# Optimization experiments

Hardware: AMD Instinct MI355X
Metric: run time of the kernel (lower is better)

The kernel has to match this reference:

```python
import jax, jax.numpy as jnp
import numpy as np

N_IN = 1024
N_OUT = 1024
BATCH = 8192
N_GRID = 10  # grid_points = linspace(-1, 1, 10); 9 segments
LN_EPS = 1e-5


def setup_inputs() -> dict:
    key = jax.random.key(0)
    k = jax.random.split(key, 6)
    return {
        "x": jax.random.normal(k[0], (BATCH, N_IN), dtype=jnp.float32),
        "weights": jax.random.normal(k[1], (N_OUT, N_IN), dtype=jnp.float32) * (1.0 / np.sqrt(N_IN)),
        "biases": jax.random.normal(k[2], (N_OUT,), dtype=jnp.float32),
        "slopes": jax.random.normal(k[3], (N_OUT, N_IN, N_GRID - 1), dtype=jnp.float32) * 0.05,
        "intercepts": jax.random.normal(k[4], (N_OUT, N_IN, N_GRID - 1), dtype=jnp.float32) * 0.05,
        "prelu_weight": jnp.full((1,), 0.25, dtype=jnp.float32),
    }


def reference(x, weights, biases, slopes, intercepts, prelu_weight):
    grid = jnp.linspace(-1.0, 1.0, N_GRID, dtype=x.dtype)
    n_seg = N_GRID - 1

    # base branch: GELU (exact, matching torch nn.GELU default) then linear
    b_out = jax.nn.gelu(x, approximate=False) @ weights.T + biases  # [B, n_out]

    # segment index per (sample, input feature)
    pos = (x[..., None] - grid) >= 0  # [B, n_in, N_GRID]
    seg = jnp.clip(jnp.sum(pos.astype(jnp.int32), axis=-1) - 1, 0, n_seg - 1)  # [B, n_in]

    # Faithful to torch.gather semantics: only slopes[:, 0, :] / intercepts[:, 0, :]
    # are read (index dim-2 has size 1 -> j==0). The piecewise sum over n_in then
    # reduces to segment-sums of x and segment counts contracted with those slices.
    onehot = jax.nn.one_hot(seg, n_seg, dtype=x.dtype)  # [B, n_in, n_seg]
    seg_x = jnp.einsum('bis,bi->bs', onehot, x)          # sum of x per segment
    seg_cnt = jnp.sum(onehot, axis=1)                    # count per segment
    slopes0 = slopes[:, 0, :]        # [n_out, n_seg]
    icpt0 = intercepts[:, 0, :]      # [n_out, n_seg]
    lin = seg_x @ slopes0.T + seg_cnt @ icpt0.T          # [B, n_out]

    y = b_out + lin
    # LayerNorm over n_out, no affine
    mu = jnp.mean(y, axis=-1, keepdims=True)
    var = jnp.mean(jnp.square(y - mu), axis=-1, keepdims=True)
    yn = (y - mu) * jax.lax.rsqrt(var + LN_EPS)
    # PReLU with single shared weight
    return jnp.where(yn >= 0, yn, prelu_weight * yn)
```

## Files before the change

### kernel.cpp

```cpp
#include <hip/hip_runtime.h>
#include <hip/hip_fp8.h>

#define N_IN 1024
#define N_OUT 1024
#define BATCHN 8192

typedef __attribute__((ext_vector_type(4))) int intx4;
typedef __attribute__((ext_vector_type(8))) int intx8;
typedef __attribute__((ext_vector_type(16))) float floatx16;

__device__ __forceinline__ unsigned int pk4_e4m3(float a, float b, float c,
                                                 float d) {
  int w = __builtin_amdgcn_cvt_pk_fp8_f32(a, b, 0, false);
  w = __builtin_amdgcn_cvt_pk_fp8_f32(c, d, w, true);
  return (unsigned int)w;
}
__device__ __forceinline__ float gelu_fast(float v) {
  float e = __builtin_amdgcn_exp2f(-2.4554443f * v);
  return v * __builtin_amdgcn_rcpf(1.0f + e);
}

__global__ __launch_bounds__(256) void prep_w(const float* __restrict__ W,
                                              unsigned char* __restrict__ Wb8,
                                              const float* __restrict__ slopes,
                                              const float* __restrict__ icpts,
                                              float* __restrict__ slt,
                                              float* __restrict__ ict) {
  const int b = blockIdx.x, t = threadIdx.x;
  if (b < N_OUT) {
    const int o = b;
    float4 v = ((const float4*)(W + o * N_IN))[t];
    unsigned int pk =
        pk4_e4m3(v.x * 16.0f, v.y * 16.0f, v.z * 16.0f, v.w * 16.0f);
    const int kc = t >> 4;
    const int lh = (t >> 3) & 1;
    const int sec = (t >> 2) & 1;
    const int off = (t & 3) * 4;
    const int lane = lh * 32 + (o & 31);
    *(unsigned int*)(Wb8 + kc * 65536 + (o >> 5) * 2048 + sec * 1024 +
                     lane * 16 + off) = pk;
  } else {
    const int gb = b - N_OUT;
    const int o = gb * 16 + (t >> 4);
    const int s = t & 15;
    if (s < 9) {
      slt[s * N_OUT + o] = slopes[(long)o * 9216 + s];
      ict[s * N_OUT + o] = icpts[(long)o * 9216 + s];
    }
  }
}

__global__ __launch_bounds__(1024) void fused(const float* __restrict__ x,
                                              const unsigned char* __restrict__ Wb8,
                                              const float* __restrict__ biases,
                                              const float* __restrict__ slt,
                                              const float* __restrict__ ict,
                                              const float* __restrict__ prelu_w,
                                              float* __restrict__ out) {
  __shared__ unsigned char lA[32 * 1024];
  __shared__ float2 seg2[32][12];
  __shared__ float2 red[16][32];
  __shared__ float2 rowstat[32];

  const int t = threadIdx.x;
  const int lane = t & 63, w = t >> 6;
  const int l31 = lane & 31, lh = lane >> 5;
  const int r0 = blockIdx.x * 32;

  for (int jr = 0; jr < 2; ++jr) {
    const int rl = 2 * w + jr;
    const float* xr = x + (r0 + rl) * N_IN;
    unsigned int* lrow = (unsigned int*)(lA + rl * 1024);
    const int sw = rl & 7;
    float cum[8], cumx[8], totx = 0.f;
#pragma unroll
    for (int s = 0; s < 8; ++s) { cum[s] = 0.f; cumx[s] = 0.f; }
#pragma unroll
    for (int jc = 0; jc < 4; ++jc) {
      float4 v4 = ((const float4*)xr)[lane + 64 * jc];
      float vs[4] = {v4.x, v4.y, v4.z, v4.w};
      float gs[4];
#pragma unroll
      for (int e = 0; e < 4; ++e) {
        float v = vs[e];
        gs[e] = gelu_fast(v) * 4.0f;
        totx += v;
#pragma unroll
        for (int k = 0; k < 8; ++k) {
          bool m = v >= (-1.0f + (float)(k + 1) * (2.0f / 9.0f));
          cum[k] += m ? 1.0f : 0.0f;
          cumx[k] += m ? v : 0.0f;
        }
      }
      const unsigned int pk = pk4_e4m3(gs[0], gs[1], gs[2], gs[3]);
      const int d = lane + 64 * jc;
      lrow[(((d >> 2) ^ sw) << 2) | (d & 3)] = pk;
    }
#pragma unroll
    for (int off = 32; off > 0; off >>= 1) {
      totx += __shfl_xor(totx, off);
#pragma unroll
      for (int s = 0; s < 8; ++s) {
        cum[s] += __shfl_xor(cum[s], off);
        cumx[s] += __shfl_xor(cumx[s], off);
      }
    }
    if (lane == 0) {
      seg2[rl][0] = make_float2(totx - cumx[0], 1024.f - cum[0]);
#pragma unroll
      for (int s = 1; s < 8; ++s)
        seg2[rl][s] = make_float2(cumx[s - 1] - cumx[s], cum[s - 1] - cum[s]);
      seg2[rl][8] = make_float2(cumx[7], cum[7]);
    }
  }
  __syncthreads();

  const int nb = w * 64;
  floatx16 acc[2] = {};
  const unsigned char* aRow = lA + l31 * 1024;
  const int asw = l31 & 7;
  const unsigned char* bBase = Wb8 + (w * 2) * 2048 + lane * 16;

#define LOAD_A(ko, AF)                                                         \
  {                                                                            \
    const int c0 = ((ko) >> 4) + lh * 2;                                       \
    intx4 lo = *(const intx4*)(aRow + ((c0 ^ asw) << 4));                      \
    intx4 hi = *(const intx4*)(aRow + (((c0 + 1) ^ asw) << 4));                \
    AF[0] = lo[0]; AF[1] = lo[1]; AF[2] = lo[2]; AF[3] = lo[3];                \
    AF[4] = hi[0]; AF[5] = hi[1]; AF[6] = hi[2]; AF[7] = hi[3];                \
  }
#define LOAD_B(kc, ni, BF)                                                     \
  {                                                                            \
    const unsigned char* bp = bBase + (kc) * 65536 + (ni) * 2048;              \
    intx4 lo = *(const intx4*)bp;                                              \
    intx4 hi = *(const intx4*)(bp + 1024);                                     \
    BF[0] = lo[0]; BF[1] = lo[1]; BF[2] = lo[2]; BF[3] = lo[3];                \
    BF[4] = hi[0]; BF[5] = hi[1]; BF[6] = hi[2]; BF[7] = hi[3];                \
  }

  const int rot = ((blockIdx.x >> 3) & 7) * 2;
  for (int kt0 = 0; kt0 < 16; kt0 += 2) {
    const int kt = (kt0 + rot) & 15;
    intx8 a0, a1, b0[2], b1[2];
    LOAD_A(kt * 64, a0);
    LOAD_A(kt * 64 + 64, a1);
#pragma unroll
    for (int ni = 0; ni < 2; ++ni) LOAD_B(kt, ni, b0[ni]);
#pragma unroll
    for (int ni = 0; ni < 2; ++ni) LOAD_B(kt + 1, ni, b1[ni]);
    __builtin_amdgcn_s_setprio(1);
#pragma unroll
    for (int ni = 0; ni < 2; ++ni)
      acc[ni] = __builtin_amdgcn_mfma_scale_f32_32x32x64_f8f6f4(
          a0, b0[ni], acc[ni], 0, 0, 0, 0x7D7D7D7Du , 0,
          0x7B7B7B7Bu );
#pragma unroll
    for (int ni = 0; ni < 2; ++ni)
      acc[ni] = __builtin_amdgcn_mfma_scale_f32_32x32x64_f8f6f4(
          a1, b1[ni], acc[ni], 0, 0, 0, 0x7D7D7D7Du, 0, 0x7B7B7B7Bu);
    __builtin_amdgcn_s_setprio(0);
  }

  float bb[2], cs[2][9], ci[2][9];
#pragma unroll
  for (int ni = 0; ni < 2; ++ni) {
    const int c = nb + ni * 32 + l31;
    bb[ni] = biases[c];
#pragma unroll
    for (int s = 0; s < 9; ++s) {
      cs[ni][s] = slt[s * N_OUT + c];
      ci[ni][s] = ict[s * N_OUT + c];
    }
  }

#pragma unroll
  for (int rg = 0; rg < 16; ++rg) {
    const int rl = (rg & 3) + 8 * (rg >> 2) + 4 * lh;
    float2 sp[9];
#pragma unroll
    for (int s = 0; s < 9; ++s) sp[s] = seg2[rl][s];
    float ssum = 0.f, qsum = 0.f;
#pragma unroll
    for (int ni = 0; ni < 2; ++ni) {
      float y = acc[ni][rg] + bb[ni];
#pragma unroll
      for (int s = 0; s < 9; ++s) y += sp[s].x * cs[ni][s] + sp[s].y * ci[ni][s];
      acc[ni][rg] = y;
      ssum += y;
      qsum += y * y;
    }
#pragma unroll
    for (int off = 16; off > 0; off >>= 1) {
      ssum += __shfl_xor(ssum, off);
      qsum += __shfl_xor(qsum, off);
    }
    if (l31 == 0) red[w][rl] = make_float2(ssum, qsum);
  }
  __syncthreads();
  if (t < 32) {
    float s = 0.f, q = 0.f;
#pragma unroll
    for (int wv = 0; wv < 16; ++wv) {
      float2 p = red[wv][t];
      s += p.x;
      q += p.y;
    }
    const float mu = s * (1.0f / 1024.0f);
    const float rstd = rsqrtf(q * (1.0f / 1024.0f) - mu * mu + 1e-5f);
    rowstat[t] = make_float2(mu, rstd);
  }
  const float pw = prelu_w[0];
  __syncthreads();
#pragma unroll
  for (int rg = 0; rg < 16; ++rg) {
    const int rl = (rg & 3) + 8 * (rg >> 2) + 4 * lh;
    const float2 ms = rowstat[rl];
    float* orow = out + (r0 + rl) * N_OUT;
#pragma unroll
    for (int ni = 0; ni < 2; ++ni) {
      float z = (acc[ni][rg] - ms.x) * ms.y;
      z = z >= 0.f ? z : pw * z;
      __builtin_nontemporal_store(z, &orow[nb + ni * 32 + l31]);
    }
  }
}

extern "C" void kernel_launch(void* const* d_in, const int* in_sizes, int n_in,
                              void* d_out, int out_size, void* d_ws, size_t ws_size,
                              hipStream_t stream) {
  const float* x = (const float*)d_in[0];
  const float* W = (const float*)d_in[1];
  const float* biases = (const float*)d_in[2];
  const float* slopes = (const float*)d_in[3];
  const float* icpts = (const float*)d_in[4];
  const float* prelu_w = (const float*)d_in[5];
  float* out = (float*)d_out;

  char* ws = (char*)d_ws;
  unsigned char* Wb8 = (unsigned char*)ws;
  float* slt = (float*)(ws + (2u << 20));
  float* ict = (float*)(ws + (2u << 20) + (64u << 10));

  prep_w<<<N_OUT + 64, 256, 0, stream>>>(W, Wb8, slopes, icpts, slt, ict);
  fused<<<BATCHN / 32, 1024, 0, stream>>>(x, Wb8, biases, slt, ict, prelu_w, out);
}
```

Before: 162.7 us.

## Software-pipeline B-fragment loads across k-steps and use ballot counts for segments

The MFMA k-loop is restructured into a register double-buffered pipeline: the first B fragments are prefetched before the barrier, and each step loads the next k-slice's B while issuing MFMAs on the current one. The rotation now has per-block granularity of one k-step and s_setprio is dropped. Segment counts are computed with wave ballot plus popcount instead of float accumulation and shuffle reductions, which cuts the VALU and shuffle work in the prologue. launch_bounds adds a min-blocks hint of 4, which may cap register use and cause spills.

```diff
diff --git a/kernel.cpp b/kernel.cpp
--- a/kernel.cpp
+++ b/kernel.cpp
@@ -50,13 +50,11 @@
   }
 }
 
-__global__ __launch_bounds__(1024) void fused(const float* __restrict__ x,
-                                              const unsigned char* __restrict__ Wb8,
-                                              const float* __restrict__ biases,
-                                              const float* __restrict__ slt,
-                                              const float* __restrict__ ict,
-                                              const float* __restrict__ prelu_w,
-                                              float* __restrict__ out) {
+__global__ __launch_bounds__(1024, 4) void fused(
+    const float* __restrict__ x, const unsigned char* __restrict__ Wb8,
+    const float* __restrict__ biases, const float* __restrict__ slt,
+    const float* __restrict__ ict, const float* __restrict__ prelu_w,
+    float* __restrict__ out) {
   __shared__ unsigned char lA[32 * 1024];
   __shared__ float2 seg2[32][12];
   __shared__ float2 red[16][32];
@@ -72,9 +70,10 @@
     const float* xr = x + (r0 + rl) * N_IN;
     unsigned int* lrow = (unsigned int*)(lA + rl * 1024);
     const int sw = rl & 7;
-    float cum[8], cumx[8], totx = 0.f;
-#pragma unroll
-    for (int s = 0; s < 8; ++s) { cum[s] = 0.f; cumx[s] = 0.f; }
+    float cumx[8], totx = 0.f;
+    unsigned int cnt[8];
+#pragma unroll
+    for (int s = 0; s < 8; ++s) { cnt[s] = 0u; cumx[s] = 0.f; }
 #pragma unroll
     for (int jc = 0; jc < 4; ++jc) {
       float4 v4 = ((const float4*)xr)[lane + 64 * jc];
@@ -88,8 +87,8 @@
 #pragma unroll
         for (int k = 0; k < 8; ++k) {
           bool m = v >= (-1.0f + (float)(k + 1) * (2.0f / 9.0f));
-          cum[k] += m ? 1.0f : 0.0f;
           cumx[k] += m ? v : 0.0f;
+          cnt[k] += (unsigned int)__popcll(__ballot(m));
         }
       }
       const unsigned int pk = pk4_e4m3(gs[0], gs[1], gs[2], gs[3]);
@@ -100,20 +99,17 @@
     for (int off = 32; off > 0; off >>= 1) {
       totx += __shfl_xor(totx, off);
 #pragma unroll
-      for (int s = 0; s < 8; ++s) {
-        cum[s] += __shfl_xor(cum[s], off);
-        cumx[s] += __shfl_xor(cumx[s], off);
-      }
+      for (int s = 0; s < 8; ++s) cumx[s] += __shfl_xor(cumx[s], off);
     }
     if (lane == 0) {
-      seg2[rl][0] = make_float2(totx - cumx[0], 1024.f - cum[0]);
+      seg2[rl][0] = make_float2(totx - cumx[0], (float)(1024 - (int)cnt[0]));
 #pragma unroll
       for (int s = 1; s < 8; ++s)
-        seg2[rl][s] = make_float2(cumx[s - 1] - cumx[s], cum[s - 1] - cum[s]);
-      seg2[rl][8] = make_float2(cumx[7], cum[7]);
-    }
-  }
-  __syncthreads();
+        seg2[rl][s] = make_float2(cumx[s - 1] - cumx[s],
+                                  (float)((int)cnt[s - 1] - (int)cnt[s]));
+      seg2[rl][8] = make_float2(cumx[7], (float)cnt[7]);
+    }
+  }
 
   const int nb = w * 64;
   floatx16 acc[2] = {};
@@ -137,28 +133,35 @@
     BF[0] = lo[0]; BF[1] = lo[1]; BF[2] = lo[2]; BF[3] = lo[3];                \
     BF[4] = hi[0]; BF[5] = hi[1]; BF[6] = hi[2]; BF[7] = hi[3];                \
   }
-
-  const int rot = ((blockIdx.x >> 3) & 7) * 2;
-  for (int kt0 = 0; kt0 < 16; kt0 += 2) {
-    const int kt = (kt0 + rot) & 15;
-    intx8 a0, a1, b0[2], b1[2];
-    LOAD_A(kt * 64, a0);
-    LOAD_A(kt * 64 + 64, a1);
-#pragma unroll
-    for (int ni = 0; ni < 2; ++ni) LOAD_B(kt, ni, b0[ni]);
-#pragma unroll
-    for (int ni = 0; ni < 2; ++ni) LOAD_B(kt + 1, ni, b1[ni]);
-    __builtin_amdgcn_s_setprio(1);
-#pragma unroll
-    for (int ni = 0; ni < 2; ++ni)
-      acc[ni] = __builtin_amdgcn_mfma_scale_f32_32x32x64_f8f6f4(
-          a0, b0[ni], acc[ni], 0, 0, 0, 0x7D7D7D7Du , 0,
-          0x7B7B7B7Bu );
-#pragma unroll
-    for (int ni = 0; ni < 2; ++ni)
-      acc[ni] = __builtin_amdgcn_mfma_scale_f32_32x32x64_f8f6f4(
-          a1, b1[ni], acc[ni], 0, 0, 0, 0x7D7D7D7Du, 0, 0x7B7B7B7Bu);
-    __builtin_amdgcn_s_setprio(0);
+#define MFMA(AF, BF, C)                                                        \
+  __builtin_amdgcn_mfma_scale_f32_32x32x64_f8f6f4(                             \
+      AF, BF, C, 0, 0, 0, 0x7D7D7D7Du , 0, 0x7B7B7B7Bu )
+
+  const int rot = (blockIdx.x >> 3) & 15;
+  intx8 a0, a1, bA0, bA1, bB0, bB1;
+  {
+    const int k0 = rot;
+    LOAD_B(k0, 0, bA0);
+    LOAD_B(k0, 1, bA1);
+  }
+  __syncthreads();
+#pragma unroll
+  for (int j = 0; j < 16; j += 2) {
+    const int k0 = (j + rot) & 15;
+    const int k1 = (j + 1 + rot) & 15;
+    const int k2 = (j + 2 + rot) & 15;
+    LOAD_A(k0 * 64, a0);
+    LOAD_B(k1, 0, bB0);
+    LOAD_B(k1, 1, bB1);
+    acc[0] = MFMA(a0, bA0, acc[0]);
+    acc[1] = MFMA(a0, bA1, acc[1]);
+    LOAD_A(k1 * 64, a1);
+    if (j < 14) {
+      LOAD_B(k2, 0, bA0);
+      LOAD_B(k2, 1, bA1);
+    }
+    acc[0] = MFMA(a1, bB0, acc[0]);
+    acc[1] = MFMA(a1, bB1, acc[1]);
   }
 
   float bb[2], cs[2][9], ci[2][9];
```

Result: slower. 167.0 us (+2.6%).

## Move x GELU/fp8 quantization and segment stats into prep kernel, async-load into GEMM

Applied to the files above, without the earlier changes.

The per-row GELU, fp8 packing and segment statistics move out of the fused GEMM kernel into the prep kernel, which runs with many small blocks and writes fp8 activations and segment sums to workspace. The GEMM kernel then copies its A tile straight into LDS with global_load_lds and reads the precomputed segment stats. Segment counts now use ballot/popcount instead of per-lane float accumulation plus shuffles. The aim is to raise parallelism for the elementwise phase and shorten the prologue of the 1024-thread GEMM blocks, at the cost of an extra global round trip of about 8 MB of fp8 activations.

```diff
diff --git a/kernel.cpp b/kernel.cpp
--- a/kernel.cpp
+++ b/kernel.cpp
@@ -20,15 +20,68 @@
   return v * __builtin_amdgcn_rcpf(1.0f + e);
 }
 
-__global__ __launch_bounds__(256) void prep_w(const float* __restrict__ W,
-                                              unsigned char* __restrict__ Wb8,
-                                              const float* __restrict__ slopes,
-                                              const float* __restrict__ icpts,
-                                              float* __restrict__ slt,
-                                              float* __restrict__ ict) {
+#define ASYNC_CP16(gp, lp)                                                     \
+  __builtin_amdgcn_global_load_lds(                                            \
+      (const __attribute__((address_space(1))) unsigned int*)(gp),             \
+      (__attribute__((address_space(3))) unsigned int*)(lp), 16, 0, 0)
+
+__global__ __launch_bounds__(256) void prep_all(const float* __restrict__ x,
+                                                unsigned char* __restrict__ g8,
+                                                float2* __restrict__ seg2g,
+                                                const float* __restrict__ W,
+                                                unsigned char* __restrict__ Wb8,
+                                                const float* __restrict__ slopes,
+                                                const float* __restrict__ icpts,
+                                                float* __restrict__ slt,
+                                                float* __restrict__ ict) {
   const int b = blockIdx.x, t = threadIdx.x;
-  if (b < N_OUT) {
-    const int o = b;
+  if (b < BATCHN / 4) {
+    const int lane = t & 63, w = t >> 6;
+    const int r = b * 4 + w;
+    const float* xr = x + (long)r * N_IN;
+    unsigned int* grow = (unsigned int*)(g8 + (long)r * N_IN);
+    const int sw = r & 7;
+    float cumx[8], totx = 0.f;
+    unsigned int cnt[8];
+#pragma unroll
+    for (int s = 0; s < 8; ++s) { cnt[s] = 0u; cumx[s] = 0.f; }
+#pragma unroll
+    for (int jc = 0; jc < 4; ++jc) {
+      float4 v4 = ((const float4*)xr)[lane + 64 * jc];
+      float vs[4] = {v4.x, v4.y, v4.z, v4.w};
+      float gs[4];
+#pragma unroll
+      for (int e = 0; e < 4; ++e) {
+        float v = vs[e];
+        gs[e] = gelu_fast(v) * 4.0f;
+        totx += v;
+#pragma unroll
+        for (int k = 0; k < 8; ++k) {
+          bool m = v >= (-1.0f + (float)(k + 1) * (2.0f / 9.0f));
+          cumx[k] += m ? v : 0.0f;
+          cnt[k] += (unsigned int)__popcll(__ballot(m));
+        }
+      }
+      const unsigned int pk = pk4_e4m3(gs[0], gs[1], gs[2], gs[3]);
+      const int d = lane + 64 * jc;
+      grow[(((d >> 2) ^ sw) << 2) | (d & 3)] = pk;
+    }
+#pragma unroll
+    for (int off = 32; off > 0; off >>= 1) {
+      totx += __shfl_xor(totx, off);
+#pragma unroll
+      for (int s = 0; s < 8; ++s) cumx[s] += __shfl_xor(cumx[s], off);
+    }
+    if (lane == 0) {
+      seg2g[r * 9 + 0] = make_float2(totx - cumx[0], (float)(1024 - (int)cnt[0]));
+#pragma unroll
+      for (int s = 1; s < 8; ++s)
+        seg2g[r * 9 + s] = make_float2(cumx[s - 1] - cumx[s],
+                                       (float)((int)cnt[s - 1] - (int)cnt[s]));
+      seg2g[r * 9 + 8] = make_float2(cumx[7], (float)cnt[7]);
+    }
+  } else if (b < BATCHN / 4 + N_OUT) {
+    const int o = b - BATCHN / 4;
     float4 v = ((const float4*)(W + o * N_IN))[t];
     unsigned int pk =
         pk4_e4m3(v.x * 16.0f, v.y * 16.0f, v.z * 16.0f, v.w * 16.0f);
@@ -40,7 +93,7 @@
     *(unsigned int*)(Wb8 + kc * 65536 + (o >> 5) * 2048 + sec * 1024 +
                      lane * 16 + off) = pk;
   } else {
-    const int gb = b - N_OUT;
+    const int gb = b - (BATCHN / 4 + N_OUT);
     const int o = gb * 16 + (t >> 4);
     const int s = t & 15;
     if (s < 9) {
@@ -50,15 +103,13 @@
   }
 }
 
-__global__ __launch_bounds__(1024) void fused(const float* __restrict__ x,
-                                              const unsigned char* __restrict__ Wb8,
-                                              const float* __restrict__ biases,
-                                              const float* __restrict__ slt,
-                                              const float* __restrict__ ict,
-                                              const float* __restrict__ prelu_w,
-                                              float* __restrict__ out) {
+__global__ __launch_bounds__(1024) void gemm_ln(
+    const unsigned char* __restrict__ g8, const unsigned char* __restrict__ Wb8,
+    const float* __restrict__ biases, const float* __restrict__ slt,
+    const float* __restrict__ ict, const float* __restrict__ prelu_w,
+    const float2* __restrict__ seg2g, float* __restrict__ out) {
   __shared__ unsigned char lA[32 * 1024];
-  __shared__ float2 seg2[32][12];
+  __shared__ float2 seg2f[288];
   __shared__ float2 red[16][32];
   __shared__ float2 rowstat[32];
 
@@ -67,52 +118,12 @@
   const int l31 = lane & 31, lh = lane >> 5;
   const int r0 = blockIdx.x * 32;
 
-  for (int jr = 0; jr < 2; ++jr) {
-    const int rl = 2 * w + jr;
-    const float* xr = x + (r0 + rl) * N_IN;
-    unsigned int* lrow = (unsigned int*)(lA + rl * 1024);
-    const int sw = rl & 7;
-    float cum[8], cumx[8], totx = 0.f;
-#pragma unroll
-    for (int s = 0; s < 8; ++s) { cum[s] = 0.f; cumx[s] = 0.f; }
-#pragma unroll
-    for (int jc = 0; jc < 4; ++jc) {
-      float4 v4 = ((const float4*)xr)[lane + 64 * jc];
-      float vs[4] = {v4.x, v4.y, v4.z, v4.w};
-      float gs[4];
-#pragma unroll
-      for (int e = 0; e < 4; ++e) {
-        float v = vs[e];
-        gs[e] = gelu_fast(v) * 4.0f;
-        totx += v;
-#pragma unroll
-        for (int k = 0; k < 8; ++k) {
-          bool m = v >= (-1.0f + (float)(k + 1) * (2.0f / 9.0f));
-          cum[k] += m ? 1.0f : 0.0f;
-          cumx[k] += m ? v : 0.0f;
-        }
-      }
-      const unsigned int pk = pk4_e4m3(gs[0], gs[1], gs[2], gs[3]);
-      const int d = lane + 64 * jc;
-      lrow[(((d >> 2) ^ sw) << 2) | (d & 3)] = pk;
-    }
-#pragma unroll
-    for (int off = 32; off > 0; off >>= 1) {
-      totx += __shfl_xor(totx, off);
-#pragma unroll
-      for (int s = 0; s < 8; ++s) {
-        cum[s] += __shfl_xor(cum[s], off);
-        cumx[s] += __shfl_xor(cumx[s], off);
-      }
-    }
-    if (lane == 0) {
-      seg2[rl][0] = make_float2(totx - cumx[0], 1024.f - cum[0]);
-#pragma unroll
-      for (int s = 1; s < 8; ++s)
-        seg2[rl][s] = make_float2(cumx[s - 1] - cumx[s], cum[s - 1] - cum[s]);
-      seg2[rl][8] = make_float2(cumx[7], cum[7]);
-    }
-  }
+#pragma unroll
+  for (int j = 0; j < 2; ++j) {
+    const int sg = t + 1024 * j;
+    ASYNC_CP16(g8 + (long)r0 * 1024 + sg * 16, &lA[sg * 16]);
+  }
+  if (t < 288) seg2f[t] = seg2g[r0 * 9 + t];
   __syncthreads();
 
   const int nb = w * 64;
@@ -178,7 +189,7 @@
     const int rl = (rg & 3) + 8 * (rg >> 2) + 4 * lh;
     float2 sp[9];
 #pragma unroll
-    for (int s = 0; s < 9; ++s) sp[s] = seg2[rl][s];
+    for (int s = 0; s < 9; ++s) sp[s] = seg2f[rl * 9 + s];
     float ssum = 0.f, qsum = 0.f;
 #pragma unroll
     for (int ni = 0; ni < 2; ++ni) {
@@ -240,7 +251,11 @@
   unsigned char* Wb8 = (unsigned char*)ws;
   float* slt = (float*)(ws + (2u << 20));
   float* ict = (float*)(ws + (2u << 20) + (64u << 10));
-
-  prep_w<<<N_OUT + 64, 256, 0, stream>>>(W, Wb8, slopes, icpts, slt, ict);
-  fused<<<BATCHN / 32, 1024, 0, stream>>>(x, Wb8, biases, slt, ict, prelu_w, out);
-}
+  unsigned char* g8 = (unsigned char*)(ws + (4u << 20));
+  float2* seg2g = (float2*)(ws + (12u << 20));
+
+  prep_all<<<BATCHN / 4 + N_OUT + 64, 256, 0, stream>>>(
+      x, g8, seg2g, W, Wb8, slopes, icpts, slt, ict);
+  gemm_ln<<<BATCHN / 32, 1024, 0, stream>>>(g8, Wb8, biases, slt, ict, prelu_w,
+                                            seg2g, out);
+}
```

After: 165.8 us. About the same (+1.9%).
